# Kernel optimization log

Hardware: AMD Instinct MI355X
Metric: run time of the kernel (lower is better)

Reference implementation:

```python
import jax, jax.numpy as jnp
import numpy as np

KSIZE = 3
KN = (KSIZE - 1) // 2  # 1
TEMP = 50.0


def _extract_patches(x, same_pad):
    """TF tf.image.extract_patches ordering: per location, (dy, dx, channel).
    x: [b,H,W,d] -> [b,h,w,9*d] (h=H,w=W if same_pad else H-2,W-2)."""
    if same_pad:
        x = jnp.pad(x, ((0, 0), (KN, KN), (KN, KN), (0, 0)))
    b, Hp, Wp, d = x.shape
    h, w = Hp - 2 * KN, Wp - 2 * KN
    slices = [x[:, dy:dy + h, dx:dx + w, :]
              for dy in range(KSIZE) for dx in range(KSIZE)]
    return jnp.concatenate(slices, axis=-1)


def setup_inputs() -> dict:
    key = jax.random.key(0)
    k1, k2, k3 = jax.random.split(key, 3)
    b, h, w, dims = 4, 48, 48, 64
    g_in = jax.random.normal(k1, (b, h, w, dims), dtype=jnp.float32)
    # binary inpainting mask (1 = known background, 0 = hole)
    mask = (jax.random.uniform(k2, (b, h, w, 1)) > 0.5).astype(jnp.float32)
    W2 = jax.random.normal(k3, (2 * dims, dims), dtype=jnp.float32) / np.sqrt(2.0 * dims)
    b2 = jnp.zeros((dims,), dtype=jnp.float32)
    return {"g_in": g_in, "mask": mask, "W2": W2, "b2": b2}


def reference(g_in, mask, W2, b2):
    b, h, w, dims = g_in.shape
    c = (h - 2 * KN) * (w - 2 * KN)

    mask_r = mask  # already (h,w,1); broadcasts over dims (== tile)
    bg = g_in * mask_r

    # p1: VALID 3x3 patches of bg -> dynamic kernels, [b, c, 9*dims]
    p1 = _extract_patches(bg, same_pad=False).reshape(b, c, KSIZE * KSIZE * dims)
    # p2: SAME 3x3 patches of g_in, [b, h, w, 9*dims]
    p2 = _extract_patches(g_in, same_pad=True)

    # cross-correlation: conv2d(ft, k1) == per-location dot with each bg patch
    CS = jnp.einsum('byxk,bjk->byxj', p2, p1)              # [b,h,w,c]
    k1d = jnp.sum(p1 * p1, axis=2)                          # [b,c]
    wwd = jnp.sum(p2 * p2, axis=3, keepdims=True)           # [b,h,w,1]
    DS1 = k1d[:, None, None, :] + wwd - 2.0 * CS            # squared distances
    mu = jnp.mean(DS1, axis=3, keepdims=True)
    sd = jnp.std(DS1, axis=3, keepdims=True)                # population std (tf.math.reduce_std)
    DS2 = -jnp.tanh((DS1 - mu) / sd)
    CA = jax.nn.softmax(TEMP * DS2, axis=-1)                # [b,h,w,c]

    # transposed conv aggregation with per-sample kernels k2[b,j,dy,dx,ch]
    k2 = p1.reshape(b, c, KSIZE, KSIZE, dims)
    CA_pad = jnp.pad(CA, ((0, 0), (KN, KN), (KN, KN), (0, 0)))
    acl = jnp.zeros((b, h, w, dims), dtype=g_in.dtype)
    for dy in range(KSIZE):
        for dx in range(KSIZE):
            win = CA_pad[:, 2 * KN - dy:2 * KN - dy + h, 2 * KN - dx:2 * KN - dx + w, :]
            acl = acl + jnp.einsum('byxj,bjd->byxd', win, k2[:, :, dy, dx, :])
    acl = acl / 9.0

    ACL = bg + acl * (1.0 - mask_r)
    con1 = jnp.concatenate([g_in, ACL], axis=3)             # [b,h,w,2*dims]
    return jax.nn.elu(jnp.einsum('byxk,kd->byxd', con1, W2) + b2)
```

## Files before the change

kernel.cpp:

```cpp
#include <hip/hip_runtime.h>
#include <hip/hip_fp16.h>
#include <math.h>

#define BB 4
#define HH 48
#define WW 48
#define DD 64
#define CH 46
#define CWp 46
#define CC (CH*CWp)
#define KK 576
#define HWp (HH*WW)
#define KPAD 2176
#define KSPLIT0 1088

typedef __attribute__((ext_vector_type(8))) short short8;
typedef __attribute__((ext_vector_type(4))) float float4v;

#define OFFB_P1H  ((size_t)0)
#define OFFB_P2H  ((size_t)9750528)
#define OFFB_P1T  ((size_t)20367360)
#define OFFB_K1D  ((size_t)30394368)
#define OFFB_S    ((size_t)30428224)
#define OFFB_AGG0 ((size_t)70536256)
#define OFFB_AGG1 ((size_t)81153088)

__device__ __forceinline__ ushort f2bf(float x) {
    unsigned u = __float_as_uint(x);
    return (ushort)((u + 0x7FFFu + ((u >> 16) & 1u)) >> 16);
}

__device__ __forceinline__ float waveReduceSum(float x) {
#pragma unroll
    for (int o = 32; o > 0; o >>= 1) x += __shfl_down(x, o, 64);
    return x;
}

__device__ __forceinline__ float blockReduceSum(float x, float* sm) {
#pragma unroll
    for (int o = 32; o > 0; o >>= 1) x += __shfl_down(x, o, 64);
    int lane = threadIdx.x & 63, w = threadIdx.x >> 6;
    __syncthreads();
    if (lane == 0) sm[w] = x;
    __syncthreads();
    return sm[0] + sm[1] + sm[2] + sm[3];
}

__device__ __forceinline__ float fast_tanh(float z) {
    float e = __expf(2.f * z);
    return 1.f - 2.f / (e + 1.f);
}

typedef __attribute__((address_space(3))) void lds_void_t;
typedef __attribute__((address_space(1))) void gmem_void_t;
__device__ __forceinline__ void gld16(const ushort* g, ushort* lds) {
    __builtin_amdgcn_global_load_lds((gmem_void_t*)g, (lds_void_t*)lds, 16, 0, 0);
}

__global__ __launch_bounds__(256) void build_patches(const float* __restrict__ g,
                                                     const float* __restrict__ mask,
                                                     ushort* __restrict__ p2h,
                                                     ushort* __restrict__ p1h,
                                                     float* __restrict__ k1d) {
    int w = threadIdx.x >> 6, c = threadIdx.x & 63;
    if (blockIdx.x < (BB * HWp / 4)) {
        int pix = blockIdx.x * 4 + w;
        int b = pix / HWp, yx = pix % HWp;
        int y = yx / WW, x = yx % WW;
        const float* gb = g + (size_t)b * HWp * DD;
        ushort* dst = p2h + (size_t)pix * KK;
#pragma unroll
        for (int dy = 0; dy < 3; dy++) {
#pragma unroll
            for (int dx = 0; dx < 3; dx++) {
                int yy = y + dy - 1, xx = x + dx - 1;
                float v = (yy >= 0 && yy < HH && xx >= 0 && xx < WW)
                              ? gb[((size_t)yy * WW + xx) * DD + c] : 0.f;
                dst[(dy * 3 + dx) * DD + c] = f2bf(v);
            }
        }
    } else {
        int j = (blockIdx.x - BB * HWp / 4) * 4 + w;
        int b = j / CC, jj = j % CC;
        int jy = jj / CWp, jx = jj % CWp;
        const float* gb = g + (size_t)b * HWp * DD;
        const float* mb = mask + (size_t)b * HWp;
        ushort* dst = p1h + (size_t)j * KK;
        float ss = 0.f;
#pragma unroll
        for (int dy = 0; dy < 3; dy++) {
#pragma unroll
            for (int dx = 0; dx < 3; dx++) {
                int p = (jy + dy) * WW + (jx + dx);
                float v = gb[(size_t)p * DD + c] * mb[p];
                dst[(dy * 3 + dx) * DD + c] = f2bf(v);
                ss += v * v;
            }
        }
        ss = waveReduceSum(ss);
        if (c == 0) k1d[j] = ss;
    }
}

__global__ __launch_bounds__(256) void transpose_p1(const ushort* __restrict__ p1h,
                                                    ushort* __restrict__ p1t) {
    __shared__ ushort T[64 * 65];
    int b = blockIdx.z;
    int j0 = blockIdx.x * 64;
    int c0 = blockIdx.y * 64;
    const ushort* src = p1h + (size_t)b * CC * KK;
    ushort* dst = p1t + (size_t)b * KK * KPAD;
    int t = threadIdx.x;
#pragma unroll
    for (int pass = 0; pass < 2; pass++) {
        int v = t + pass * 256;
        int r = v >> 3, c8 = (v & 7) * 8;
        int j = j0 + r;
        uint4 d = make_uint4(0, 0, 0, 0);
        if (j < CC) d = *(const uint4*)(src + (size_t)j * KK + c0 + c8);
        ushort tmp[8];
        *(uint4*)tmp = d;
#pragma unroll
        for (int u = 0; u < 8; u++) T[r * 65 + c8 + u] = tmp[u];
    }
    __syncthreads();
#pragma unroll
    for (int pass = 0; pass < 2; pass++) {
        int v = t + pass * 256;
        int cr = v >> 3, j8 = (v & 7) * 8;
        ushort tmp[8];
#pragma unroll
        for (int u = 0; u < 8; u++) tmp[u] = T[(j8 + u) * 65 + cr];
        *(uint4*)(dst + (size_t)(c0 + cr) * KPAD + j0 + j8) = *(uint4*)tmp;
    }
}

template <int NF, bool NMASK>
__device__ __forceinline__ void gemm_tile_db(const ushort* __restrict__ Ab,
                                             const ushort* __restrict__ Bb,
                                             int lda, int ldb, int kb, int ke,
                                             int Nrem,
                                             ushort* As, ushort* Bs,
                                             float4v (&acc)[4][NF]) {
    constexpr int NBI = NF / 2;
    constexpr int BBUF = 2048 * NBI;
    int tid = threadIdx.x;
    int l = tid & 63, w = tid >> 6;
    int quad = l >> 4, l15 = l & 15;
    int sw8 = (l15 >> 1) & 3;
    int wm = (w >> 1) * 64, wn = (w & 1) * (NF * 16);
    int rowInC = l >> 2;
    int cSw = (l & 3) ^ ((l >> 3) & 3);

#pragma unroll
    for (int i = 0; i < 2; i++) {
        int rg = w * 2 + i;
        gld16(Ab + (size_t)(rg * 16 + rowInC) * lda + kb + cSw * 8, As + rg * 512);
    }
#pragma unroll
    for (int i = 0; i < NBI; i++) {
        int rg = w * NBI + i;
        int r = rg * 16 + rowInC;
        if (!NMASK || r < Nrem)
            gld16(Bb + (size_t)r * ldb + kb + cSw * 8, Bs + rg * 512);
    }

    int buf = 0;
    for (int k0 = kb; k0 < ke; k0 += 32) {
        __syncthreads();
        int nb = buf ^ 1;
        if (k0 + 32 < ke) {
#pragma unroll
            for (int i = 0; i < 2; i++) {
                int rg = w * 2 + i;
                gld16(Ab + (size_t)(rg * 16 + rowInC) * lda + (k0 + 32) + cSw * 8,
                      As + nb * 4096 + rg * 512);
            }
#pragma unroll
            for (int i = 0; i < NBI; i++) {
                int rg = w * NBI + i;
                int r = rg * 16 + rowInC;
                if (!NMASK || r < Nrem)
                    gld16(Bb + (size_t)r * ldb + (k0 + 32) + cSw * 8,
                          Bs + nb * BBUF + rg * 512);
            }
        }
        const ushort* Ax = As + buf * 4096;
        const ushort* Bx = Bs + buf * BBUF;
        short8 af[4], bf[NF];
#pragma unroll
        for (int i = 0; i < 4; i++)
            af[i] = *(const short8*)&Ax[(wm + i * 16 + l15) * 32 + ((quad ^ sw8)) * 8];
#pragma unroll
        for (int j = 0; j < NF; j++)
            bf[j] = *(const short8*)&Bx[(wn + j * 16 + l15) * 32 + ((quad ^ sw8)) * 8];
#pragma unroll
        for (int i = 0; i < 4; i++)
#pragma unroll
            for (int j = 0; j < NF; j++)
                acc[i][j] = __builtin_amdgcn_mfma_f32_16x16x32_bf16(af[i], bf[j], acc[i][j], 0, 0, 0);
        buf = nb;
    }
}

__global__ __launch_bounds__(256) void gemm1_nt(const ushort* __restrict__ A,
                                                const ushort* __restrict__ Bt,
                                                __half* __restrict__ Cout) {
    __shared__ ushort As[2 * 4096];
    __shared__ ushort Bs[2 * 4096];
    int i0 = blockIdx.x;
    int b = (i0 & 7) >> 1;
    int tile = ((i0 >> 3) << 1) | (i0 & 1);
    int ty = tile / 17, tx = tile - ty * 17;
    int m0 = ty * 128, n0 = tx * 128;
    const ushort* Ab = A + (size_t)b * HWp * KK + (size_t)m0 * KK;
    const ushort* Bb = Bt + (size_t)b * CC * KK + (size_t)n0 * KK;
    float4v acc[4][4];
#pragma unroll
    for (int i = 0; i < 4; i++)
#pragma unroll
        for (int j = 0; j < 4; j++) acc[i][j] = (float4v){0.f, 0.f, 0.f, 0.f};

    gemm_tile_db<4, true>(Ab, Bb, KK, KK, 0, KK, CC - n0, As, Bs, acc);

    int tid = threadIdx.x;
    int lane = tid & 63, wid = tid >> 6;
    int quad = lane >> 4, l15 = lane & 15;
    int wm = (wid >> 1) * 64, wn = (wid & 1) * 64;
    __half* C = Cout + (size_t)b * HWp * KPAD;
#pragma unroll
    for (int i = 0; i < 4; i++) {
#pragma unroll
        for (int j = 0; j < 4; j++) {
            int n = n0 + wn + j * 16 + l15;
            if (n < CC) {
#pragma unroll
                for (int r = 0; r < 4; r++) {
                    int m = m0 + wm + i * 16 + quad * 4 + r;
                    C[(size_t)m * KPAD + n] = __float2half(acc[i][j][r]);
                }
            }
        }
    }
}

__global__ __launch_bounds__(256) void gemm2_split(const ushort* __restrict__ A,
                                                   const ushort* __restrict__ Bt,
                                                   __half* __restrict__ agg0,
                                                   __half* __restrict__ agg1) {
    __shared__ ushort As[2 * 4096];
    __shared__ ushort Bs[2 * 6144];
    int i0 = blockIdx.x;
    int z = i0 & 7;
    int b = z >> 1, split = z & 1;
    int tile = i0 >> 3;
    int ty = tile / 3, tx = tile - ty * 3;
    int m0 = ty * 128, n0 = tx * 192;
    const ushort* Ab = A + (size_t)b * HWp * KPAD + (size_t)m0 * KPAD;
    const ushort* Bb = Bt + (size_t)b * KK * KPAD + (size_t)n0 * KPAD;
    float4v acc[4][6];
#pragma unroll
    for (int i = 0; i < 4; i++)
#pragma unroll
        for (int j = 0; j < 6; j++) acc[i][j] = (float4v){0.f, 0.f, 0.f, 0.f};

    gemm_tile_db<6, false>(Ab, Bb, KPAD, KPAD, split ? KSPLIT0 : 0,
                           split ? KPAD : KSPLIT0, 192, As, Bs, acc);

    int tid = threadIdx.x;
    int lane = tid & 63, wid = tid >> 6;
    int quad = lane >> 4, l15 = lane & 15;
    int wm = (wid >> 1) * 64, wn = (wid & 1) * 96;
    __half* C = (split ? agg1 : agg0) + (size_t)b * HWp * KK;
#pragma unroll
    for (int i = 0; i < 4; i++) {
#pragma unroll
        for (int j = 0; j < 6; j++) {
            int n = n0 + wn + j * 16 + l15;
#pragma unroll
            for (int r = 0; r < 4; r++) {
                int m = m0 + wm + i * 16 + quad * 4 + r;
                C[(size_t)m * KK + n] = __float2half(acc[i][j][r]);
            }
        }
    }
}

__global__ __launch_bounds__(256) void rowsoft(void* __restrict__ Sbase,
                                               const float* __restrict__ k1d) {
    __shared__ float sm[4];
    size_t row = blockIdx.x;
    int b = (int)(row / HWp);
    const __half* p = (const __half*)Sbase + row * KPAD;
    ushort* wout = (ushort*)Sbase + row * KPAD;
    const float* k1 = k1d + (size_t)b * CC;
    int t = threadIdx.x;
    bool hasx = t < 34;

    uint4 raw = *(const uint4*)(p + t * 8);
    uint rx = hasx ? *(const uint*)(p + 2048 + t * 2) : 0u;
    float v[8], vx[2];
    {
        const __half2* h2 = (const __half2*)&raw;
#pragma unroll
        for (int i = 0; i < 4; i++) {
            float2 f = __half22float2(h2[i]);
            v[2 * i] = f.x; v[2 * i + 1] = f.y;
        }
        __half2 hx = *(__half2*)&rx;
        float2 fx = __half22float2(hx);
        vx[0] = fx.x; vx[1] = fx.y;
    }
    {
        const float* kp = k1 + t * 8;
#pragma unroll
        for (int i = 0; i < 8; i++) v[i] = kp[i] - 2.f * v[i];
        if (hasx) {
            vx[0] = k1[2048 + t * 2] - 2.f * vx[0];
            vx[1] = k1[2048 + t * 2 + 1] - 2.f * vx[1];
        }
    }
    float s = 0.f;
#pragma unroll
    for (int i = 0; i < 8; i++) s += v[i];
    if (hasx) s += vx[0] + vx[1];
    s = blockReduceSum(s, sm);
    float mu = s / (float)CC;
    float vs = 0.f;
#pragma unroll
    for (int i = 0; i < 8; i++) { float d = v[i] - mu; vs += d * d; }
    if (hasx) { float d0 = vx[0] - mu, d1 = vx[1] - mu; vs += d0 * d0 + d1 * d1; }
    vs = blockReduceSum(vs, sm);
    float inv_sd = 1.f / sqrtf(vs / (float)CC);
    float es = 0.f;
#pragma unroll
    for (int i = 0; i < 8; i++) {
        v[i] = __expf(-50.f * fast_tanh((v[i] - mu) * inv_sd));
        es += v[i];
    }
    if (hasx) {
        vx[0] = __expf(-50.f * fast_tanh((vx[0] - mu) * inv_sd));
        vx[1] = __expf(-50.f * fast_tanh((vx[1] - mu) * inv_sd));
        es += vx[0] + vx[1];
    }
    es = blockReduceSum(es, sm);
    float invz = 1.f / es;

    ushort o[8];
#pragma unroll
    for (int i = 0; i < 8; i++) o[i] = f2bf(v[i] * invz);
    *(uint4*)(wout + t * 8) = *(const uint4*)o;
    if (hasx) {
        ushort ox[2] = { f2bf(vx[0] * invz), f2bf(vx[1] * invz) };
        *(uint*)(wout + 2048 + t * 2) = *(const uint*)ox;
    } else {
        *(uint*)(wout + CC + 2 * (t - 34)) = 0u;
    }
}

__global__ __launch_bounds__(256) void final_k(const float* __restrict__ g,
                                               const float* __restrict__ mask,
                                               const __half* __restrict__ agg0,
                                               const __half* __restrict__ agg1,
                                               const float* __restrict__ W2,
                                               const float* __restrict__ b2,
                                               float* __restrict__ out) {
    int w = threadIdx.x >> 6, d = threadIdx.x & 63;
    int pix = blockIdx.x * 4 + w;
    int b = pix / HWp, yx = pix % HWp;
    int y = yx / WW, x = yx % WW;

    __shared__ float con1[4][128];
    float acl = 0.f;
#pragma unroll
    for (int dy = 0; dy < 3; dy++) {
#pragma unroll
        for (int dx = 0; dx < 3; dx++) {
            int yy = y + 1 - dy, xx = x + 1 - dx;
            if (yy >= 0 && yy < HH && xx >= 0 && xx < WW) {
                size_t off = ((size_t)(b * HWp + yy * WW + xx)) * KK + (dy * 3 + dx) * DD + d;
                acl += __half2float(agg0[off]) + __half2float(agg1[off]);
            }
        }
    }
    float m = mask[pix];
    float gv = g[(size_t)pix * DD + d];
    float bgv = gv * m;
    float ACL = bgv + (acl / 9.f) * (1.f - m);
    con1[w][d] = gv;
    con1[w][64 + d] = ACL;
    __syncthreads();
    float accv = b2[d];
#pragma unroll 8
    for (int k = 0; k < 128; k++) accv = fmaf(con1[w][k], W2[k * 64 + d], accv);
    out[(size_t)pix * DD + d] = accv > 0.f ? accv : expm1f(accv);
}

extern "C" void kernel_launch(void* const* d_in, const int* in_sizes, int n_in,
                              void* d_out, int out_size, void* d_ws, size_t ws_size,
                              hipStream_t stream) {
    const float* g    = (const float*)d_in[0];
    const float* mask = (const float*)d_in[1];
    const float* W2   = (const float*)d_in[2];
    const float* b2   = (const float*)d_in[3];
    float* out = (float*)d_out;
    char* ws = (char*)d_ws;

    ushort* p1h  = (ushort*)(ws + OFFB_P1H);
    ushort* p2h  = (ushort*)(ws + OFFB_P2H);
    ushort* p1t  = (ushort*)(ws + OFFB_P1T);
    float*  k1d  = (float*) (ws + OFFB_K1D);
    void*   S    = (void*)  (ws + OFFB_S);
    __half* agg0 = (__half*)(ws + OFFB_AGG0);
    __half* agg1 = (__half*)(ws + OFFB_AGG1);

    build_patches<<<BB * HWp / 4 + BB * CC / 4, 256, 0, stream>>>(g, mask, p2h, p1h, k1d);
    transpose_p1<<<dim3(34, 9, BB), 256, 0, stream>>>(p1h, p1t);

    gemm1_nt<<<dim3(1224), 256, 0, stream>>>(p2h, p1h, (__half*)S);

    rowsoft<<<BB * HWp, 256, 0, stream>>>(S, k1d);

    gemm2_split<<<dim3(432), 256, 0, stream>>>((const ushort*)S, p1t, agg0, agg1);

    final_k<<<BB * HWp / 4, 256, 0, stream>>>(g, mask, agg0, agg1, W2, b2, out);
}
```

Baseline: 192.8 us.

## Gather im2col patches on the fly in GEMM1 from padded bf16 images

```diff
diff --git a/kernel.cpp b/kernel.cpp
--- a/kernel.cpp
+++ b/kernel.cpp
@@ -13,17 +13,20 @@
 #define HWp (HH*WW)
 #define KPAD 2176
 #define KSPLIT0 1088
+#define PW 50
+#define PP (PW*PW)
 
 typedef __attribute__((ext_vector_type(8))) short short8;
 typedef __attribute__((ext_vector_type(4))) float float4v;
 
-#define OFFB_P1H  ((size_t)0)
-#define OFFB_P2H  ((size_t)9750528)
-#define OFFB_P1T  ((size_t)20367360)
-#define OFFB_K1D  ((size_t)30394368)
-#define OFFB_S    ((size_t)30428224)
-#define OFFB_AGG0 ((size_t)70536256)
-#define OFFB_AGG1 ((size_t)81153088)
+#define OFFB_GPAD  ((size_t)0)
+#define OFFB_BGPAD ((size_t)1280000)
+#define OFFB_E     ((size_t)2560000)
+#define OFFB_K1D   ((size_t)2596864)
+#define OFFB_P1T   ((size_t)2630720)
+#define OFFB_S     ((size_t)12657728)
+#define OFFB_AGG0  ((size_t)52765760)
+#define OFFB_AGG1  ((size_t)63382592)
 
 __device__ __forceinline__ ushort f2bf(float x) {
     unsigned u = __float_as_uint(x);
@@ -57,81 +60,174 @@
     __builtin_amdgcn_global_load_lds((gmem_void_t*)g, (lds_void_t*)lds, 16, 0, 0);
 }
 
-__global__ __launch_bounds__(256) void build_patches(const float* __restrict__ g,
-                                                     const float* __restrict__ mask,
-                                                     ushort* __restrict__ p2h,
-                                                     ushort* __restrict__ p1h,
+__global__ __launch_bounds__(256) void build_pads(const float* __restrict__ g,
+                                                  const float* __restrict__ mask,
+                                                  ushort* __restrict__ gpad,
+                                                  ushort* __restrict__ bgpad,
+                                                  float* __restrict__ e) {
+    int w = threadIdx.x >> 6, c = threadIdx.x & 63;
+    int q4 = blockIdx.x * 4 + w;
+    int b = q4 / PP, q = q4 % PP;
+    int yp = q / PW, xp = q % PW;
+    size_t o = (size_t)q4 * DD + c;
+    if (yp >= 1 && yp <= HH && xp >= 1 && xp <= WW) {
+        int pix = (yp - 1) * WW + (xp - 1);
+        float gv = g[((size_t)b * HWp + pix) * DD + c];
+        float m  = mask[(size_t)b * HWp + pix];
+        float bgv = gv * m;
+        gpad[o]  = f2bf(gv);
+        bgpad[o] = f2bf(bgv);
+        float ss = waveReduceSum(bgv * bgv);
+        if (c == 0) e[b * HWp + pix] = ss;
+    } else {
+        gpad[o] = 0;
+        bgpad[o] = 0;
+    }
+}
+
+__global__ __launch_bounds__(256) void build_p1t_k1d(const ushort* __restrict__ bgpad,
+                                                     const float* __restrict__ e,
+                                                     ushort* __restrict__ p1t,
                                                      float* __restrict__ k1d) {
-    int w = threadIdx.x >> 6, c = threadIdx.x & 63;
-    if (blockIdx.x < (BB * HWp / 4)) {
-        int pix = blockIdx.x * 4 + w;
-        int b = pix / HWp, yx = pix % HWp;
-        int y = yx / WW, x = yx % WW;
-        const float* gb = g + (size_t)b * HWp * DD;
-        ushort* dst = p2h + (size_t)pix * KK;
-#pragma unroll
-        for (int dy = 0; dy < 3; dy++) {
-#pragma unroll
-            for (int dx = 0; dx < 3; dx++) {
-                int yy = y + dy - 1, xx = x + dx - 1;
-                float v = (yy >= 0 && yy < HH && xx >= 0 && xx < WW)
-                              ? gb[((size_t)yy * WW + xx) * DD + c] : 0.f;
-                dst[(dy * 3 + dx) * DD + c] = f2bf(v);
-            }
+    int t = threadIdx.x;
+    if (blockIdx.x < BB * KK) {
+        int rowid = blockIdx.x;
+        int b = rowid / KK, n = rowid % KK;
+        int d9 = n >> 6, c = n & 63;
+        int dy = d9 / 3, dx = d9 - dy * 3;
+        const ushort* src = bgpad + (size_t)b * PP * DD + c;
+        ushort* dst = p1t + (size_t)rowid * KPAD;
+#pragma unroll
+        for (int pass = 0; pass < 2; pass++) {
+            int j0;
+            if (pass == 0) j0 = t * 8;
+            else { if (t >= 16) break; j0 = 2048 + t * 8; }
+            ushort v[8];
+#pragma unroll
+            for (int u = 0; u < 8; u++) {
+                int j = j0 + u;
+                ushort val = 0;
+                if (j < CC) {
+                    int jy = j / CWp, jx = j - jy * CWp;
+                    val = src[(size_t)((jy + dy + 1) * PW + (jx + dx + 1)) * DD];
+                }
+                v[u] = val;
+            }
+            *(uint4*)(dst + j0) = *(const uint4*)v;
         }
     } else {
-        int j = (blockIdx.x - BB * HWp / 4) * 4 + w;
-        int b = j / CC, jj = j % CC;
-        int jy = jj / CWp, jx = jj % CWp;
-        const float* gb = g + (size_t)b * HWp * DD;
-        const float* mb = mask + (size_t)b * HWp;
-        ushort* dst = p1h + (size_t)j * KK;
-        float ss = 0.f;
-#pragma unroll
-        for (int dy = 0; dy < 3; dy++) {
-#pragma unroll
-            for (int dx = 0; dx < 3; dx++) {
-                int p = (jy + dy) * WW + (jx + dx);
-                float v = gb[(size_t)p * DD + c] * mb[p];
-                dst[(dy * 3 + dx) * DD + c] = f2bf(v);
-                ss += v * v;
-            }
-        }
-        ss = waveReduceSum(ss);
-        if (c == 0) k1d[j] = ss;
-    }
-}
-
-__global__ __launch_bounds__(256) void transpose_p1(const ushort* __restrict__ p1h,
-                                                    ushort* __restrict__ p1t) {
-    __shared__ ushort T[64 * 65];
-    int b = blockIdx.z;
-    int j0 = blockIdx.x * 64;
-    int c0 = blockIdx.y * 64;
-    const ushort* src = p1h + (size_t)b * CC * KK;
-    ushort* dst = p1t + (size_t)b * KK * KPAD;
-    int t = threadIdx.x;
-#pragma unroll
-    for (int pass = 0; pass < 2; pass++) {
-        int v = t + pass * 256;
-        int r = v >> 3, c8 = (v & 7) * 8;
-        int j = j0 + r;
-        uint4 d = make_uint4(0, 0, 0, 0);
-        if (j < CC) d = *(const uint4*)(src + (size_t)j * KK + c0 + c8);
-        ushort tmp[8];
-        *(uint4*)tmp = d;
-#pragma unroll
-        for (int u = 0; u < 8; u++) T[r * 65 + c8 + u] = tmp[u];
-    }
-    __syncthreads();
-#pragma unroll
-    for (int pass = 0; pass < 2; pass++) {
-        int v = t + pass * 256;
-        int cr = v >> 3, j8 = (v & 7) * 8;
-        ushort tmp[8];
-#pragma unroll
-        for (int u = 0; u < 8; u++) tmp[u] = T[(j8 + u) * 65 + cr];
-        *(uint4*)(dst + (size_t)(c0 + cr) * KPAD + j0 + j8) = *(uint4*)tmp;
+        int jg = (blockIdx.x - BB * KK) * 256 + t;
+        if (jg < BB * CC) {
+            int b = jg / CC, j = jg % CC;
+            int jy = j / CWp, jx = j - jy * CWp;
+            const float* eb = e + b * HWp + jy * WW + jx;
+            float s = 0.f;
+#pragma unroll
+            for (int dy = 0; dy < 3; dy++)
+#pragma unroll
+                for (int dx = 0; dx < 3; dx++) s += eb[dy * WW + dx];
+            k1d[jg] = s;
+        }
+    }
+}
+
+__global__ __launch_bounds__(256) void gemm1_nt(const ushort* __restrict__ gpad,
+                                                const ushort* __restrict__ bgpad,
+                                                __half* __restrict__ Cout) {
+    __shared__ ushort As[2 * 4096];
+    __shared__ ushort Bs[2 * 4096];
+    int i0 = blockIdx.x;
+    int b = (i0 & 7) >> 1;
+    int tile = ((i0 >> 3) << 1) | (i0 & 1);
+    int ty = tile / 17, tx = tile - ty * 17;
+    int m0 = ty * 128, n0 = tx * 128;
+    const ushort* Ag = gpad + (size_t)b * PP * DD;
+    const ushort* Bg = bgpad + (size_t)b * PP * DD;
+
+    int tid = threadIdx.x;
+    int l = tid & 63, w = tid >> 6;
+    int quad = l >> 4, l15 = l & 15;
+    int sw8 = (l15 >> 1) & 3;
+    int wm = (w >> 1) * 64, wn = (w & 1) * 64;
+    int rowInC = l >> 2;
+    int cSw = (l & 3) ^ ((l >> 3) & 3);
+
+    int baseA[2], baseB[2];
+    bool vB[2];
+#pragma unroll
+    for (int i = 0; i < 2; i++) {
+        int rg = w * 2 + i;
+        int r = rg * 16 + rowInC;
+        int p = m0 + r;
+        int y = p / WW, x = p - y * WW;
+        baseA[i] = (y * PW + x) * DD + cSw * 8;
+        int n = n0 + r;
+        vB[i] = (n < CC);
+        int jy = 0, jx = 0;
+        if (vB[i]) { jy = n / CWp; jx = n - jy * CWp; }
+        baseB[i] = ((jy + 1) * PW + (jx + 1)) * DD + cSw * 8;
+    }
+
+    float4v acc[4][4];
+#pragma unroll
+    for (int i = 0; i < 4; i++)
+#pragma unroll
+        for (int j = 0; j < 4; j++) acc[i][j] = (float4v){0.f, 0.f, 0.f, 0.f};
+
+#pragma unroll
+    for (int i = 0; i < 2; i++) {
+        int rg = w * 2 + i;
+        gld16(Ag + baseA[i], As + rg * 512);
+        if (vB[i]) gld16(Bg + baseB[i], Bs + rg * 512);
+    }
+
+    int buf = 0;
+    for (int k0 = 0; k0 < KK; k0 += 32) {
+        __syncthreads();
+        int nb = buf ^ 1;
+        int kn = k0 + 32;
+        if (kn < KK) {
+            int d9 = kn >> 6;
+            int dy = d9 / 3, dx = d9 - dy * 3;
+            int off = (dy * PW + dx) * DD + (kn & 63);
+#pragma unroll
+            for (int i = 0; i < 2; i++) {
+                int rg = w * 2 + i;
+                gld16(Ag + baseA[i] + off, As + nb * 4096 + rg * 512);
+                if (vB[i]) gld16(Bg + baseB[i] + off, Bs + nb * 4096 + rg * 512);
+            }
+        }
+        const ushort* Ax = As + buf * 4096;
+        const ushort* Bx = Bs + buf * 4096;
+        short8 af[4], bf[4];
+#pragma unroll
+        for (int i = 0; i < 4; i++)
+            af[i] = *(const short8*)&Ax[(wm + i * 16 + l15) * 32 + ((quad ^ sw8)) * 8];
+#pragma unroll
+        for (int j = 0; j < 4; j++)
+            bf[j] = *(const short8*)&Bx[(wn + j * 16 + l15) * 32 + ((quad ^ sw8)) * 8];
+#pragma unroll
+        for (int i = 0; i < 4; i++)
+#pragma unroll
+            for (int j = 0; j < 4; j++)
+                acc[i][j] = __builtin_amdgcn_mfma_f32_16x16x32_bf16(af[i], bf[j], acc[i][j], 0, 0, 0);
+        buf = nb;
+    }
+
+    __half* C = Cout + (size_t)b * HWp * KPAD;
+#pragma unroll
+    for (int i = 0; i < 4; i++) {
+#pragma unroll
+        for (int j = 0; j < 4; j++) {
+            int n = n0 + wn + j * 16 + l15;
+            if (n < CC) {
+#pragma unroll
+                for (int r = 0; r < 4; r++) {
+                    int m = m0 + wm + i * 16 + quad * 4 + r;
+                    C[(size_t)m * KPAD + n] = __float2half(acc[i][j][r]);
+                }
+            }
+        }
     }
 }
 
@@ -203,47 +299,6 @@
     }
 }
 
-__global__ __launch_bounds__(256) void gemm1_nt(const ushort* __restrict__ A,
-                                                const ushort* __restrict__ Bt,
-                                                __half* __restrict__ Cout) {
-    __shared__ ushort As[2 * 4096];
-    __shared__ ushort Bs[2 * 4096];
-    int i0 = blockIdx.x;
-    int b = (i0 & 7) >> 1;
-    int tile = ((i0 >> 3) << 1) | (i0 & 1);
-    int ty = tile / 17, tx = tile - ty * 17;
-    int m0 = ty * 128, n0 = tx * 128;
-    const ushort* Ab = A + (size_t)b * HWp * KK + (size_t)m0 * KK;
-    const ushort* Bb = Bt + (size_t)b * CC * KK + (size_t)n0 * KK;
-    float4v acc[4][4];
-#pragma unroll
-    for (int i = 0; i < 4; i++)
-#pragma unroll
-        for (int j = 0; j < 4; j++) acc[i][j] = (float4v){0.f, 0.f, 0.f, 0.f};
-
-    gemm_tile_db<4, true>(Ab, Bb, KK, KK, 0, KK, CC - n0, As, Bs, acc);
-
-    int tid = threadIdx.x;
-    int lane = tid & 63, wid = tid >> 6;
-    int quad = lane >> 4, l15 = lane & 15;
-    int wm = (wid >> 1) * 64, wn = (wid & 1) * 64;
-    __half* C = Cout + (size_t)b * HWp * KPAD;
-#pragma unroll
-    for (int i = 0; i < 4; i++) {
-#pragma unroll
-        for (int j = 0; j < 4; j++) {
-            int n = n0 + wn + j * 16 + l15;
-            if (n < CC) {
-#pragma unroll
-                for (int r = 0; r < 4; r++) {
-                    int m = m0 + wm + i * 16 + quad * 4 + r;
-                    C[(size_t)m * KPAD + n] = __float2half(acc[i][j][r]);
-                }
-            }
-        }
-    }
-}
-
 __global__ __launch_bounds__(256) void gemm2_split(const ushort* __restrict__ A,
                                                    const ushort* __restrict__ Bt,
                                                    __half* __restrict__ agg0,
@@ -406,18 +461,19 @@
     float* out = (float*)d_out;
     char* ws = (char*)d_ws;
 
-    ushort* p1h  = (ushort*)(ws + OFFB_P1H);
-    ushort* p2h  = (ushort*)(ws + OFFB_P2H);
-    ushort* p1t  = (ushort*)(ws + OFFB_P1T);
-    float*  k1d  = (float*) (ws + OFFB_K1D);
-    void*   S    = (void*)  (ws + OFFB_S);
-    __half* agg0 = (__half*)(ws + OFFB_AGG0);
-    __half* agg1 = (__half*)(ws + OFFB_AGG1);
-
-    build_patches<<<BB * HWp / 4 + BB * CC / 4, 256, 0, stream>>>(g, mask, p2h, p1h, k1d);
-    transpose_p1<<<dim3(34, 9, BB), 256, 0, stream>>>(p1h, p1t);
-
-    gemm1_nt<<<dim3(1224), 256, 0, stream>>>(p2h, p1h, (__half*)S);
+    ushort* gpad  = (ushort*)(ws + OFFB_GPAD);
+    ushort* bgpad = (ushort*)(ws + OFFB_BGPAD);
+    float*  e     = (float*) (ws + OFFB_E);
+    float*  k1d   = (float*) (ws + OFFB_K1D);
+    ushort* p1t   = (ushort*)(ws + OFFB_P1T);
+    void*   S     = (void*)  (ws + OFFB_S);
+    __half* agg0  = (__half*)(ws + OFFB_AGG0);
+    __half* agg1  = (__half*)(ws + OFFB_AGG1);
+
+    build_pads<<<BB * PP / 4, 256, 0, stream>>>(g, mask, gpad, bgpad, e);
+    build_p1t_k1d<<<BB * KK + 34, 256, 0, stream>>>(bgpad, e, p1t, k1d);
+
+    gemm1_nt<<<dim3(1224), 256, 0, stream>>>(gpad, bgpad, (__half*)S);
 
     rowsoft<<<BB * HWp, 256, 0, stream>>>(S, k1d);
 
```

New measurement: 205.4 us. +6.5%, slower.
